# Optimization experiments

Hardware: AMD Instinct MI355X
Metric: run time of the kernel (lower is better)

The kernel has to match this reference:

```python
import jax, jax.numpy as jnp
import numpy as np

SMOOTH = 1.0
MAX_DIST = 10


def _neighbor_conv(x):
    # 3x3 ones kernel with zero center, padding=1 (NCHW, C=1)
    k = jnp.ones((1, 1, 3, 3), x.dtype).at[0, 0, 1, 1].set(0.0)
    return jax.lax.conv_general_dilated(
        x, k, window_strides=(1, 1), padding=[(1, 1), (1, 1)],
        dimension_numbers=('NCHW', 'OIHW', 'NCHW'))


def _analyze_skeleton(skel):
    n = _neighbor_conv(skel)
    on = skel > 0.5
    endpoints = ((n == 1) & on).astype(skel.dtype)
    midpoints = ((n == 2) & on).astype(skel.dtype)
    junctions = ((n > 2) & on).astype(skel.dtype)
    return endpoints, midpoints, junctions


def _iou(p, g):
    inter = jnp.sum(p * g, axis=(2, 3))
    union = jnp.sum(p, axis=(2, 3)) + jnp.sum(g, axis=(2, 3)) - inter
    return (inter + SMOOTH) / (union + SMOOTH)


def _structural_similarity(pred_skel, gt_skel):
    pe, pm, pj = _analyze_skeleton(pred_skel)
    ge, gm, gj = _analyze_skeleton(gt_skel)
    e_iou, m_iou, j_iou = _iou(pe, ge), _iou(pm, gm), _iou(pj, gj)
    ge_c = jnp.sum(ge, axis=(2, 3))
    gj_c = jnp.sum(gj, axis=(2, 3))
    gm_c = jnp.sum(gm, axis=(2, 3))
    total = ge_c + gj_c + gm_c + SMOOTH
    loss = 1.0 - ((ge_c / total) * e_iou + (gj_c / total) * j_iou + (gm_c / total) * m_iou)
    return loss.mean()


def _maxpool3(x):
    return jax.lax.reduce_window(
        x, -jnp.inf, jax.lax.max,
        window_dimensions=(1, 1, 3, 3), window_strides=(1, 1, 1, 1),
        padding=[(0, 0), (0, 0), (1, 1), (1, 1)])


def _distance_approximation(target, reference):
    # Fixed MAX_DIST iterations; identical math to the torch early-exit loop
    # because new_points requires ~found_mask (no distance is overwritten).
    tgt_on = target > 0.5

    def step(carry, d):
        dilated, found, dist = carry
        dilated = _maxpool3(dilated)
        new = (dilated > 0.5) & tgt_on & (~found)
        dist = dist + d.astype(dist.dtype) * new.astype(dist.dtype)
        return (dilated, found | new, dist), None

    init = (reference, jnp.zeros(target.shape, bool), jnp.zeros_like(target))
    (_, found, dist), _ = jax.lax.scan(step, init, jnp.arange(1, MAX_DIST + 1, dtype=jnp.int32))
    unfound = tgt_on & (~found)
    dist = dist + jnp.asarray(MAX_DIST, dist.dtype) * unfound.astype(dist.dtype)
    total_points = jnp.sum(tgt_on.astype(dist.dtype), axis=(2, 3))
    return jnp.sum(dist, axis=(2, 3)) / (total_points + SMOOTH)


def _medial_axis_distance(pred_skel, gt_skel):
    p2g = _distance_approximation(pred_skel, gt_skel)
    g2p = _distance_approximation(gt_skel, pred_skel)
    return (((p2g + g2p) / 2.0) / MAX_DIST).mean()


def setup_inputs() -> dict:
    key = jax.random.key(0)
    k1, k2 = jax.random.split(key)
    B, C, H, W = 32, 1, 512, 512
    pred_skel = jax.random.uniform(k1, (B, C, H, W), dtype=jnp.float32)
    gt_skel = (jax.random.uniform(k2, (B, C, H, W), dtype=jnp.float32) < 0.1).astype(jnp.float32)
    return {"pred_skel": pred_skel, "gt_skel": gt_skel}


def reference(pred_skel, gt_skel):
    inter = jnp.sum(pred_skel * gt_skel, axis=(2, 3))
    psum = jnp.sum(pred_skel, axis=(2, 3))
    gsum = jnp.sum(gt_skel, axis=(2, 3))
    dice = (2.0 * inter + SMOOTH) / (psum + gsum + SMOOTH)
    dice_loss = 1.0 - dice.mean()
    structural_loss = _structural_similarity(pred_skel, gt_skel)
    medial_loss = _medial_axis_distance(pred_skel, gt_skel)
    avg_mag = (dice_loss + structural_loss + medial_loss) / 3.0
    bal_dice = dice_loss / (dice_loss + SMOOTH) * avg_mag
    bal_struct = structural_loss / (structural_loss + SMOOTH) * avg_mag
    bal_medial = medial_loss / (medial_loss + SMOOTH) * avg_mag
    return bal_dice + bal_struct + bal_medial
```

## Files before the change

### kernel.cpp

```cpp
#include <hip/hip_runtime.h>
#include <stdint.h>

#define BATCH 32
#define H 512
#define W 512
#define NACC 16
#define TH 32
#define HALO 9
#define RH (TH + 2*HALO)
#define NT 1024
#define NW (NT/64)
#define NTILE (H/TH)
#define NBLK (NTILE*BATCH)


__global__ __launch_bounds__(NT, 4) void fused_kernel(
    const float* __restrict__ pred, const float* __restrict__ gt,
    float* __restrict__ part)
{
    __shared__ uint64_t Mp[2][RH][8];
    __shared__ uint64_t Mg[2][RH][8];
    __shared__ float    EC[2][TH];
    __shared__ float    red[NW][16];

    int fid = blockIdx.x;
    int b   = fid >> 4;
    int t4  = fid & 15;
    int tile = ((t4 & 7) << 1) | (t4 >> 3);

    const float* pimg = pred + (size_t)b * H * W;
    const float* gimg = gt   + (size_t)b * H * W;
    int y0 = tile * TH;
    int tid = threadIdx.x, lane = tid & 63, wid = tid >> 6;

    for (int s = wid; s < RH * 8; s += 2 * NW) {
        int sB = s + NW;
        int rA = s >> 3, segA = s & 7;
        int rB = sB >> 3, segB = sB & 7;
        int ryA = y0 - HALO + rA, ryB = y0 - HALO + rB;
        bool okB = sB < RH * 8;
        float vpA = 0.f, vgA = 0.f, vpB = 0.f, vgB = 0.f;
        if ((unsigned)ryA < (unsigned)H) {
            int idx = ryA * W + segA * 64 + lane;
            vpA = pimg[idx]; vgA = gimg[idx];
        }
        if (okB && (unsigned)ryB < (unsigned)H) {
            int idx = ryB * W + segB * 64 + lane;
            vpB = pimg[idx]; vgB = gimg[idx];
        }
        unsigned long long mpA = __ballot(vpA > 0.5f);
        unsigned long long mgA = __ballot(vgA > 0.5f);
        if (lane == 0) { Mp[0][rA][segA] = mpA; Mg[0][rA][segA] = mgA; }
        if (okB) {
            unsigned long long mpB = __ballot(vpB > 0.5f);
            unsigned long long mgB = __ballot(vgB > 0.5f);
            if (lane == 0) { Mp[0][rB][segB] = mpB; Mg[0][rB][segB] = mgB; }
        }
    }
    if (tid < 2 * TH) {
        int c = tid >> 5, r = tid & (TH - 1);
        int y = y0 + r, col = 255 + c;
        float sum = (y > 0     ? pimg[(size_t)(y - 1) * W + col] : 0.f)
                  +              pimg[(size_t)y * W + col]
                  + (y < H - 1 ? pimg[(size_t)(y + 1) * W + col] : 0.f);
        EC[c][r] = sum;
    }
    __syncthreads();

    uint64_t Tp = 0ULL, Tg = 0ULL;
    int rT = HALO + (tid >> 3), wT = tid & 7;
    if (tid < TH * 8) { Tp = Mp[0][rT][wT]; Tg = Mg[0][rT][wT]; }
    int dcnt_p = __popcll(Tp), dcnt_g = __popcll(Tg);
    int dsum_p = dcnt_p, dsum_g = dcnt_g;

    float v0 = 0.f, v1 = 0.f;
    uint64_t cpack = 0ULL;
    {
        int qi = tid & 127, h = tid >> 7;
        int x4 = qi * 4;
        int wdx = qi >> 4;
        int ss = (qi & 15) * 4;
        int ys = y0 + h * 4;

        auto win6 = [&](int rb) -> uint32_t {
            const uint64_t* row = Mg[0][rb];
            uint64_t bm = row[wdx];
            if (ss == 0) {
                uint64_t lo = wdx ? row[wdx - 1] : 0ULL;
                return (uint32_t)(((bm << 1) | (lo >> 63)) & 0x3FULL);
            }
            uint32_t v = (uint32_t)((bm >> (ss - 1)) & 0x3FULL);
            if (ss == 60) {
                uint64_t hi = (wdx < 7) ? row[wdx + 1] : 0ULL;
                v |= ((uint32_t)hi & 1u) << 5;
            }
            return v;
        };

        int rb0 = h * 4 + HALO - 1;
        uint32_t wU = win6(rb0), wM = win6(rb0 + 1);

        float4 pm4, pc4;
        {
            bool hm = ys > 0;
            pm4 = hm ? *(const float4*)(pimg + (size_t)(ys - 1) * W + x4)
                     : make_float4(0, 0, 0, 0);
            pc4 = *(const float4*)(pimg + (size_t)ys * W + x4);
        }
        for (int r = 0; r < 4; ++r) {
            int y = ys + r;
            float4 pp4 = (y < H - 1) ? *(const float4*)(pimg + (size_t)(y + 1) * W + x4)
                                     : make_float4(0, 0, 0, 0);
            uint32_t wD = win6(rb0 + 2 + r);
            int ry = h * 4 + r;

            float ps[6];
            ps[1] = pm4.x + pc4.x + pp4.x; ps[2] = pm4.y + pc4.y + pp4.y;
            ps[3] = pm4.z + pc4.z + pp4.z; ps[4] = pm4.w + pc4.w + pp4.w;
            float psl = __shfl_up(ps[4], 1, 64);
            float psr = __shfl_down(ps[1], 1, 64);
            if (lane == 0)  psl = (qi == 0)   ? 0.f : EC[0][ry];
            if (lane == 63) psr = (qi == 127) ? 0.f : EC[1][ry];
            ps[0] = psl; ps[5] = psr;

            float pcv[4] = {pc4.x, pc4.y, pc4.z, pc4.w};
            #pragma unroll
            for (int j = 0; j < 4; ++j) {
                float np = ps[j] + ps[j + 1] + ps[j + 2] - pcv[j];
                bool pon = pcv[j] > 0.5f;
                bool pe  = pon && (np == 1.f);
                bool pmb = pon && (np == 2.f);
                bool pjb = pon && (np > 2.f);
                uint32_t n9 = ((wU >> j) & 7u) | (((wM >> j) & 7u) << 3) | (((wD >> j) & 7u) << 6);
                uint32_t cen = (wM >> (j + 1)) & 1u;
                int ng = __popc(n9) - (int)cen;
                bool gon = cen != 0u;
                bool ge  = gon && (ng == 1);
                bool gmb = gon && (ng == 2);
                bool gjb = gon && (ng > 2);
                v1 += pcv[j];
                v0 += gon ? pcv[j] : 0.f;
                cpack += (uint64_t)pe
                       | ((uint64_t)pmb << 7)
                       | ((uint64_t)pjb << 14)
                       | ((uint64_t)ge  << 21)
                       | ((uint64_t)gmb << 28)
                       | ((uint64_t)gjb << 35)
                       | ((uint64_t)(pe  && ge)  << 42)
                       | ((uint64_t)(pmb && gmb) << 49)
                       | ((uint64_t)(pjb && gjb) << 56);
            }
            pm4 = pc4; pc4 = pp4; wU = wM; wM = wD;
        }
    }

    int cur = 0;
    int half = tid >> 9;
    int t    = tid & 511;
    for (int a = 1; a <= 9; ++a) {
        int ntask = (RH - 2 * a) * 8;
        if (t < ntask) {
            int r = a + (t >> 3), w = t & 7;
            uint64_t (*Msrc)[8] = half ? Mg[cur] : Mp[cur];
            uint64_t (*Mdst)[8] = half ? Mg[cur ^ 1] : Mp[cur ^ 1];
            uint64_t X = Msrc[r - 1][w] | Msrc[r][w] | Msrc[r + 1][w];
            uint32_t lm = __shfl_up  ((uint32_t)(X >> 63), 1, 64);
            uint32_t rl = __shfl_down((uint32_t)(X & 1ULL), 1, 64);
            uint64_t Y = X | (X << 1) | (X >> 1);
            if (w > 0) Y |= (uint64_t)(lm & 1u);
            if (w < 7) Y |= ((uint64_t)(rl & 1u)) << 63;
            Mdst[r][w] = Y;
        }
        __syncthreads();
        cur ^= 1;
        if (tid < TH * 8) {
            dsum_p += __popcll(Tp & ~Mg[cur][rT][wT]);
            dsum_g += __popcll(Tg & ~Mp[cur][rT][wT]);
        }
    }

    float vals[16];
    vals[0] = v0; vals[1] = v1; vals[2] = (float)dcnt_g;
    vals[3]  = (float)((cpack      ) & 0x7F);
    vals[4]  = (float)((cpack >> 7 ) & 0x7F);
    vals[5]  = (float)((cpack >> 14) & 0x7F);
    vals[6]  = (float)((cpack >> 21) & 0x7F);
    vals[7]  = (float)((cpack >> 28) & 0x7F);
    vals[8]  = (float)((cpack >> 35) & 0x7F);
    vals[9]  = (float)((cpack >> 42) & 0x7F);
    vals[10] = (float)((cpack >> 49) & 0x7F);
    vals[11] = (float)((cpack >> 56) & 0x7F);
    vals[12] = (float)dsum_p; vals[13] = (float)dcnt_p;
    vals[14] = (float)dsum_g; vals[15] = (float)dcnt_g;
    #pragma unroll
    for (int j = 0; j < 16; ++j)
        #pragma unroll
        for (int off = 32; off; off >>= 1)
            vals[j] += __shfl_down(vals[j], off, 64);
    if (lane == 0) {
        #pragma unroll
        for (int j = 0; j < 16; ++j) red[wid][j] = vals[j];
    }
    __syncthreads();
    if (tid < 16) {
        float s = 0.f;
        #pragma unroll
        for (int wv = 0; wv < NW; ++wv) s += red[wv][tid];
        part[fid * NACC + tid] = s;
    }
}

__global__ __launch_bounds__(512) void final_kernel(
    const float* __restrict__ part, float* __restrict__ out)
{
    __shared__ float sacc[BATCH][NACC];
    __shared__ float tri[BATCH][3];
    int t = threadIdx.x;
    {
        int b = t >> 4, k = t & 15;
        float s = 0.f;
        #pragma unroll 4
        for (int j = 0; j < NTILE; ++j)
            s += part[((b << 4) + j) * NACC + k];
        sacc[b][k] = s;
    }
    __syncthreads();
    if (t < BATCH) {
        const float* a = sacc[t];
        float inter = a[0], psum = a[1], gsum = a[2];
        float dice = (2.f * inter + 1.f) / (psum + gsum + 1.f);

        float pe = a[3], pm = a[4], pj = a[5];
        float ge = a[6], gm = a[7], gj = a[8];
        float ie = a[9], im = a[10], ij = a[11];
        float e_iou = (ie + 1.f) / (pe + ge - ie + 1.f);
        float m_iou = (im + 1.f) / (pm + gm - im + 1.f);
        float j_iou = (ij + 1.f) / (pj + gj - ij + 1.f);
        float total = ge + gj + gm + 1.f;
        float sloss = 1.f - ((ge / total) * e_iou + (gj / total) * j_iou + (gm / total) * m_iou);

        float p2g = a[12] / (a[13] + 1.f);
        float g2p = a[14] / (a[15] + 1.f);
        float med = ((p2g + g2p) * 0.5f) / 10.f;
        tri[t][0] = dice; tri[t][1] = sloss; tri[t][2] = med;
    }
    __syncthreads();
    if (t == 0) {
        float dice = 0.f, sloss = 0.f, med = 0.f;
        for (int b = 0; b < BATCH; ++b) {
            dice += tri[b][0]; sloss += tri[b][1]; med += tri[b][2];
        }
        float dice_loss  = 1.f - dice / (float)BATCH;
        float structural = sloss / (float)BATCH;
        float medial     = med / (float)BATCH;
        float avg = (dice_loss + structural + medial) / 3.f;
        float r = dice_loss  / (dice_loss  + 1.f) * avg
                + structural / (structural + 1.f) * avg
                + medial     / (medial     + 1.f) * avg;
        out[0] = r;
    }
}

extern "C" void kernel_launch(void* const* d_in, const int* in_sizes, int n_in,
                              void* d_out, int out_size, void* d_ws, size_t ws_size,
                              hipStream_t stream)
{
    const float* pred = (const float*)d_in[0];
    const float* gt   = (const float*)d_in[1];
    float* part = (float*)d_ws;
    float* out  = (float*)d_out;

    fused_kernel<<<dim3(NBLK), NT, 0, stream>>>(pred, gt, part);
    final_kernel<<<1, 512, 0, stream>>>(part, out);
}
```

Before: 124.1 us.

## Replace iterative dilation with per-thread ring accumulation; halve block threads

The nine shared-memory dilation passes, each ending in a block-wide barrier, are replaced by per-thread accumulation. Each thread reads the rows at distance a above and below from the unchanged mask and widens them horizontally with doubling shifts, which builds the Chebyshev ball incrementally without any synchronisation. The block size drops from 1024 to 512 threads, so each thread does 8 rows of the structural analysis, and blocks are reordered batch-minor. This saves the barriers and double-buffered shared stores at the cost of more LDS reads and register work per thread, and halves the threads available to hide load latency.

```diff
diff --git a/kernel.cpp b/kernel.cpp
--- a/kernel.cpp
+++ b/kernel.cpp
@@ -8,7 +8,8 @@
 #define TH 32
 #define HALO 9
 #define RH (TH + 2*HALO)
-#define NT 1024
+#define NWORDS (RH*8)
+#define NT 512
 #define NW (NT/64)
 #define NTILE (H/TH)
 #define NBLK (NTILE*BATCH)
@@ -18,45 +19,46 @@
     const float* __restrict__ pred, const float* __restrict__ gt,
     float* __restrict__ part)
 {
-    __shared__ uint64_t Mp[2][RH][8];
-    __shared__ uint64_t Mg[2][RH][8];
+    __shared__ uint64_t MpS[NWORDS + 2];
+    __shared__ uint64_t MgS[NWORDS + 2];
     __shared__ float    EC[2][TH];
     __shared__ float    red[NW][16];
 
-    int fid = blockIdx.x;
-    int b   = fid >> 4;
-    int t4  = fid & 15;
-    int tile = ((t4 & 7) << 1) | (t4 >> 3);
+    uint64_t* Mp = MpS + 1;
+    uint64_t* Mg = MgS + 1;
+
+    int fid  = blockIdx.x;
+    int b    = fid & 31;
+    int tile = fid >> 5;
 
     const float* pimg = pred + (size_t)b * H * W;
     const float* gimg = gt   + (size_t)b * H * W;
     int y0 = tile * TH;
     int tid = threadIdx.x, lane = tid & 63, wid = tid >> 6;
 
-    for (int s = wid; s < RH * 8; s += 2 * NW) {
+    for (int s = wid; s < NWORDS; s += 2 * NW) {
         int sB = s + NW;
-        int rA = s >> 3, segA = s & 7;
-        int rB = sB >> 3, segB = sB & 7;
-        int ryA = y0 - HALO + rA, ryB = y0 - HALO + rB;
-        bool okB = sB < RH * 8;
+        int ryA = y0 - HALO + (s >> 3);
+        int ryB = y0 - HALO + (sB >> 3);
         float vpA = 0.f, vgA = 0.f, vpB = 0.f, vgB = 0.f;
         if ((unsigned)ryA < (unsigned)H) {
-            int idx = ryA * W + segA * 64 + lane;
-            vpA = pimg[idx]; vgA = gimg[idx];
-        }
-        if (okB && (unsigned)ryB < (unsigned)H) {
-            int idx = ryB * W + segB * 64 + lane;
-            vpB = pimg[idx]; vgB = gimg[idx];
+            int i0 = ryA * W + (s & 7) * 64 + lane;
+            vpA = pimg[i0]; vgA = gimg[i0];
+        }
+        if ((unsigned)ryB < (unsigned)H) {
+            int i1 = ryB * W + (sB & 7) * 64 + lane;
+            vpB = pimg[i1]; vgB = gimg[i1];
         }
         unsigned long long mpA = __ballot(vpA > 0.5f);
         unsigned long long mgA = __ballot(vgA > 0.5f);
-        if (lane == 0) { Mp[0][rA][segA] = mpA; Mg[0][rA][segA] = mgA; }
-        if (okB) {
-            unsigned long long mpB = __ballot(vpB > 0.5f);
-            unsigned long long mgB = __ballot(vgB > 0.5f);
-            if (lane == 0) { Mp[0][rB][segB] = mpB; Mg[0][rB][segB] = mgB; }
-        }
-    }
+        unsigned long long mpB = __ballot(vpB > 0.5f);
+        unsigned long long mgB = __ballot(vgB > 0.5f);
+        if (lane == 0) {
+            Mp[s]  = mpA; Mg[s]  = mgA;
+            Mp[sB] = mpB; Mg[sB] = mgB;
+        }
+    }
+    if (tid == 0) { MpS[0] = 0; MpS[NWORDS + 1] = 0; MgS[0] = 0; MgS[NWORDS + 1] = 0; }
     if (tid < 2 * TH) {
         int c = tid >> 5, r = tid & (TH - 1);
         int y = y0 + r, col = 255 + c;
@@ -67,12 +69,6 @@
     }
     __syncthreads();
 
-    uint64_t Tp = 0ULL, Tg = 0ULL;
-    int rT = HALO + (tid >> 3), wT = tid & 7;
-    if (tid < TH * 8) { Tp = Mp[0][rT][wT]; Tg = Mg[0][rT][wT]; }
-    int dcnt_p = __popcll(Tp), dcnt_g = __popcll(Tg);
-    int dsum_p = dcnt_p, dsum_g = dcnt_g;
-
     float v0 = 0.f, v1 = 0.f;
     uint64_t cpack = 0ULL;
     {
@@ -80,10 +76,10 @@
         int x4 = qi * 4;
         int wdx = qi >> 4;
         int ss = (qi & 15) * 4;
-        int ys = y0 + h * 4;
+        int ys = y0 + h * 8;
 
         auto win6 = [&](int rb) -> uint32_t {
-            const uint64_t* row = Mg[0][rb];
+            const uint64_t* row = &Mg[rb * 8];
             uint64_t bm = row[wdx];
             if (ss == 0) {
                 uint64_t lo = wdx ? row[wdx - 1] : 0ULL;
@@ -97,7 +93,7 @@
             return v;
         };
 
-        int rb0 = h * 4 + HALO - 1;
+        int rb0 = h * 8 + HALO - 1;
         uint32_t wU = win6(rb0), wM = win6(rb0 + 1);
 
         float4 pm4, pc4;
@@ -107,12 +103,12 @@
                      : make_float4(0, 0, 0, 0);
             pc4 = *(const float4*)(pimg + (size_t)ys * W + x4);
         }
-        for (int r = 0; r < 4; ++r) {
+        for (int r = 0; r < 8; ++r) {
             int y = ys + r;
             float4 pp4 = (y < H - 1) ? *(const float4*)(pimg + (size_t)(y + 1) * W + x4)
                                      : make_float4(0, 0, 0, 0);
             uint32_t wD = win6(rb0 + 2 + r);
-            int ry = h * 4 + r;
+            int ry = h * 8 + r;
 
             float ps[6];
             ps[1] = pm4.x + pc4.x + pp4.x; ps[2] = pm4.y + pc4.y + pp4.y;
@@ -154,33 +150,58 @@
         }
     }
 
-    int cur = 0;
-    int half = tid >> 9;
-    int t    = tid & 511;
+    bool isP = tid < 256;
+    int idx = tid & 255;
+    int o   = (HALO + (idx >> 3)) * 8 + (idx & 7);
+    int w   = idx & 7;
+    bool wL = (w > 0), wR = (w < 7);
+    const uint64_t* MT = isP ? Mp : Mg;
+    const uint64_t* MV = isP ? Mg : Mp;
+
+    uint64_t T = MT[o];
+    int dcnt = __popcll(T);
+    int dsum = dcnt;
+    uint64_t VM = MV[o];
+    uint64_t VL = wL ? MV[o - 1] : 0ULL;
+    uint64_t VR = wR ? MV[o + 1] : 0ULL;
+    uint64_t C = VM;
+
+    #pragma unroll
     for (int a = 1; a <= 9; ++a) {
-        int ntask = (RH - 2 * a) * 8;
-        if (t < ntask) {
-            int r = a + (t >> 3), w = t & 7;
-            uint64_t (*Msrc)[8] = half ? Mg[cur] : Mp[cur];
-            uint64_t (*Mdst)[8] = half ? Mg[cur ^ 1] : Mp[cur ^ 1];
-            uint64_t X = Msrc[r - 1][w] | Msrc[r][w] | Msrc[r + 1][w];
-            uint32_t lm = __shfl_up  ((uint32_t)(X >> 63), 1, 64);
-            uint32_t rl = __shfl_down((uint32_t)(X & 1ULL), 1, 64);
-            uint64_t Y = X | (X << 1) | (X >> 1);
-            if (w > 0) Y |= (uint64_t)(lm & 1u);
-            if (w < 7) Y |= ((uint64_t)(rl & 1u)) << 63;
-            Mdst[r][w] = Y;
-        }
-        __syncthreads();
-        cur ^= 1;
-        if (tid < TH * 8) {
-            dsum_p += __popcll(Tp & ~Mg[cur][rT][wT]);
-            dsum_g += __popcll(Tg & ~Mp[cur][rT][wT]);
-        }
+        int lo = o - 8 * a, hi = o + 8 * a;
+        uint64_t NM = MV[lo] | MV[hi];
+        uint64_t NL = wL ? (MV[lo - 1] | MV[hi - 1]) : 0ULL;
+        uint64_t NR = wR ? (MV[lo + 1] | MV[hi + 1]) : 0ULL;
+        uint64_t SL = NL, SM = NM, SR = NR;
+        const int m = a - 1;
+        if (m >= 1) {
+            SM |= (SM << 1) | (SM >> 1) | (SL >> 63) | (SR << 63);
+            SL |= SL << 1; SR |= SR >> 1;
+        }
+        if (m >= 2) {
+            const int s = (m == 2) ? 1 : 2;
+            SM |= (SM << s) | (SM >> s) | (SL >> (64 - s)) | (SR << (64 - s));
+            SL |= SL << s; SR |= SR >> s;
+        }
+        if (m >= 4) {
+            const int s = (m - 3 < 4) ? (m - 3) : 4;
+            SM |= (SM << s) | (SM >> s) | (SL >> (64 - s)) | (SR << (64 - s));
+            SL |= SL << s; SR |= SR >> s;
+        }
+        if (m >= 8) {
+            const int s = m - 7;
+            SM |= (SM << s) | (SM >> s) | (SL >> (64 - s)) | (SR << (64 - s));
+            SL |= SL << s; SR |= SR >> s;
+        }
+        C |= SM;
+        VL |= NL; VM |= NM; VR |= NR;
+        C |= (VM << a) | (VM >> a) | (VL >> (64 - a)) | (VR << (64 - a));
+        dsum += __popcll(T & ~C);
     }
 
     float vals[16];
-    vals[0] = v0; vals[1] = v1; vals[2] = (float)dcnt_g;
+    vals[0] = v0; vals[1] = v1;
+    vals[2]  = isP ? 0.f : (float)dcnt;
     vals[3]  = (float)((cpack      ) & 0x7F);
     vals[4]  = (float)((cpack >> 7 ) & 0x7F);
     vals[5]  = (float)((cpack >> 14) & 0x7F);
@@ -190,8 +211,10 @@
     vals[9]  = (float)((cpack >> 42) & 0x7F);
     vals[10] = (float)((cpack >> 49) & 0x7F);
     vals[11] = (float)((cpack >> 56) & 0x7F);
-    vals[12] = (float)dsum_p; vals[13] = (float)dcnt_p;
-    vals[14] = (float)dsum_g; vals[15] = (float)dcnt_g;
+    vals[12] = isP ? (float)dsum : 0.f;
+    vals[13] = isP ? (float)dcnt : 0.f;
+    vals[14] = isP ? 0.f : (float)dsum;
+    vals[15] = isP ? 0.f : (float)dcnt;
     #pragma unroll
     for (int j = 0; j < 16; ++j)
         #pragma unroll
@@ -221,7 +244,7 @@
         float s = 0.f;
         #pragma unroll 4
         for (int j = 0; j < NTILE; ++j)
-            s += part[((b << 4) + j) * NACC + k];
+            s += part[((j << 5) + b) * NACC + k];
         sacc[b][k] = s;
     }
     __syncthreads();
```

After: 126.5 us. Within noise of the previous version (+2.0%).

## Batch mask loads four-deep, move dice sums to mask phase, reorder block mapping

Applied to the files above, without the earlier changes.

The mask-building loop now issues four row-segment loads per warp before the ballots, instead of two, giving more memory-level parallelism. The dice sums (pred total and pred masked by gt) move from the classification loop into this load phase, reusing values already in registers. The first float4 prefetch for the classification stage is hoisted ahead of the EC load and barrier. Block-to-tile mapping changes so consecutive blocks cover different images at the same tile row, and the final kernel's indexing is updated to match. The risks are higher register pressure under launch bounds (1024,4) and different L2 locality across neighbouring blocks.

```diff
diff --git a/kernel.cpp b/kernel.cpp
--- a/kernel.cpp
+++ b/kernel.cpp
@@ -8,6 +8,7 @@
 #define TH 32
 #define HALO 9
 #define RH (TH + 2*HALO)
+#define NWORDS (RH*8)
 #define NT 1024
 #define NW (NT/64)
 #define NTILE (H/TH)
@@ -23,40 +24,54 @@
     __shared__ float    EC[2][TH];
     __shared__ float    red[NW][16];
 
-    int fid = blockIdx.x;
-    int b   = fid >> 4;
-    int t4  = fid & 15;
-    int tile = ((t4 & 7) << 1) | (t4 >> 3);
+    int fid  = blockIdx.x;
+    int b    = fid & 31;
+    int tile = fid >> 5;
 
     const float* pimg = pred + (size_t)b * H * W;
     const float* gimg = gt   + (size_t)b * H * W;
     int y0 = tile * TH;
     int tid = threadIdx.x, lane = tid & 63, wid = tid >> 6;
 
-    for (int s = wid; s < RH * 8; s += 2 * NW) {
-        int sB = s + NW;
-        int rA = s >> 3, segA = s & 7;
-        int rB = sB >> 3, segB = sB & 7;
-        int ryA = y0 - HALO + rA, ryB = y0 - HALO + rB;
-        bool okB = sB < RH * 8;
-        float vpA = 0.f, vgA = 0.f, vpB = 0.f, vgB = 0.f;
-        if ((unsigned)ryA < (unsigned)H) {
-            int idx = ryA * W + segA * 64 + lane;
-            vpA = pimg[idx]; vgA = gimg[idx];
-        }
-        if (okB && (unsigned)ryB < (unsigned)H) {
-            int idx = ryB * W + segB * 64 + lane;
-            vpB = pimg[idx]; vgB = gimg[idx];
-        }
-        unsigned long long mpA = __ballot(vpA > 0.5f);
-        unsigned long long mgA = __ballot(vgA > 0.5f);
-        if (lane == 0) { Mp[0][rA][segA] = mpA; Mg[0][rA][segA] = mgA; }
-        if (okB) {
-            unsigned long long mpB = __ballot(vpB > 0.5f);
-            unsigned long long mgB = __ballot(vgB > 0.5f);
-            if (lane == 0) { Mp[0][rB][segB] = mpB; Mg[0][rB][segB] = mgB; }
-        }
-    }
+    uint64_t* Mp0 = &Mp[0][0][0];
+    uint64_t* Mg0 = &Mg[0][0][0];
+
+    float v0 = 0.f, v1 = 0.f;
+    for (int s0 = wid; s0 < NWORDS; s0 += 4 * NW) {
+        float vp[4], vg[4];
+        #pragma unroll
+        for (int u = 0; u < 4; ++u) {
+            int s = s0 + u * NW;
+            vp[u] = 0.f; vg[u] = 0.f;
+            int ry = y0 - HALO + (s >> 3);
+            if (s < NWORDS && (unsigned)ry < (unsigned)H) {
+                int i0 = ry * W + (s & 7) * 64 + lane;
+                vp[u] = pimg[i0]; vg[u] = gimg[i0];
+            }
+        }
+        #pragma unroll
+        for (int u = 0; u < 4; ++u) {
+            int s = s0 + u * NW;
+            if (s < NWORDS) {
+                unsigned long long mp = __ballot(vp[u] > 0.5f);
+                unsigned long long mg = __ballot(vg[u] > 0.5f);
+                if (lane == 0) { Mp0[s] = mp; Mg0[s] = mg; }
+                int r = s >> 3;
+                if (r >= HALO && r < HALO + TH) {
+                    v1 += vp[u];
+                    v0 += (vg[u] > 0.5f) ? vp[u] : 0.f;
+                }
+            }
+        }
+    }
+
+    int qi = tid & 127, h = tid >> 7;
+    int x4 = qi * 4;
+    int ys = y0 + h * 4;
+    float4 pm4 = (ys > 0) ? *(const float4*)(pimg + (size_t)(ys - 1) * W + x4)
+                          : make_float4(0, 0, 0, 0);
+    float4 pc4 = *(const float4*)(pimg + (size_t)ys * W + x4);
+
     if (tid < 2 * TH) {
         int c = tid >> 5, r = tid & (TH - 1);
         int y = y0 + r, col = 255 + c;
@@ -73,14 +88,10 @@
     int dcnt_p = __popcll(Tp), dcnt_g = __popcll(Tg);
     int dsum_p = dcnt_p, dsum_g = dcnt_g;
 
-    float v0 = 0.f, v1 = 0.f;
     uint64_t cpack = 0ULL;
     {
-        int qi = tid & 127, h = tid >> 7;
-        int x4 = qi * 4;
         int wdx = qi >> 4;
         int ss = (qi & 15) * 4;
-        int ys = y0 + h * 4;
 
         auto win6 = [&](int rb) -> uint32_t {
             const uint64_t* row = Mg[0][rb];
@@ -100,13 +111,6 @@
         int rb0 = h * 4 + HALO - 1;
         uint32_t wU = win6(rb0), wM = win6(rb0 + 1);
 
-        float4 pm4, pc4;
-        {
-            bool hm = ys > 0;
-            pm4 = hm ? *(const float4*)(pimg + (size_t)(ys - 1) * W + x4)
-                     : make_float4(0, 0, 0, 0);
-            pc4 = *(const float4*)(pimg + (size_t)ys * W + x4);
-        }
         for (int r = 0; r < 4; ++r) {
             int y = ys + r;
             float4 pp4 = (y < H - 1) ? *(const float4*)(pimg + (size_t)(y + 1) * W + x4)
@@ -138,8 +142,6 @@
                 bool ge  = gon && (ng == 1);
                 bool gmb = gon && (ng == 2);
                 bool gjb = gon && (ng > 2);
-                v1 += pcv[j];
-                v0 += gon ? pcv[j] : 0.f;
                 cpack += (uint64_t)pe
                        | ((uint64_t)pmb << 7)
                        | ((uint64_t)pjb << 14)
@@ -180,7 +182,8 @@
     }
 
     float vals[16];
-    vals[0] = v0; vals[1] = v1; vals[2] = (float)dcnt_g;
+    vals[0] = v0; vals[1] = v1;
+    vals[2]  = (float)dcnt_g;
     vals[3]  = (float)((cpack      ) & 0x7F);
     vals[4]  = (float)((cpack >> 7 ) & 0x7F);
     vals[5]  = (float)((cpack >> 14) & 0x7F);
@@ -221,7 +224,7 @@
         float s = 0.f;
         #pragma unroll 4
         for (int j = 0; j < NTILE; ++j)
-            s += part[((b << 4) + j) * NACC + k];
+            s += part[((j << 5) + b) * NACC + k];
         sacc[b][k] = s;
     }
     __syncthreads();
```

After: 125.8 us. About the same (+1.4%).
